# Optimization experiments

Measured on AMD Instinct MI355X. Metric: run time of the kernel, lower is better.

## Reference

```python
import jax, jax.numpy as jnp
import numpy as np

HALF_LOG_2PI = 0.9189385332046727  # 0.5*log(2*pi)


def _sum_layer(prod, logits):
    # prod: [B, R, KK] child log-probs; logits: [R, KK, K] unnormalized sum weights
    W = jax.nn.softmax(logits, axis=1)            # normalized mixture weights
    m = jnp.max(prod, axis=-1, keepdims=True)     # stable logsumexp via einsum
    e = jnp.exp(prod - m)                         # [B, R, KK]
    s = jnp.einsum('brc,rck->brk', e, W)          # [B, R, K]
    return jnp.log(s) + m


def setup_inputs() -> dict:
    key = jax.random.key(0)
    ks = jax.random.split(key, 12)
    B, F, K = 8192, 256, 8
    inp = {
        'x': jax.random.normal(ks[0], (B, F), dtype=jnp.float32),
        'mu': jax.random.normal(ks[1], (F, K), dtype=jnp.float32),
        'log_sigma': jax.random.uniform(ks[2], (F, K), dtype=jnp.float32),
    }
    R = F // 2
    for i in range(8):
        inp['w%d' % i] = jax.random.normal(ks[3 + i], (R, K * K, K), dtype=jnp.float32)
        R //= 2
    inp['root_w'] = jax.random.normal(ks[11], (K,), dtype=jnp.float32)
    return inp


def reference(x, mu, log_sigma, w0, w1, w2, w3, w4, w5, w6, w7, root_w):
    # Gaussian leaf log-probs: [B, F, K]
    z = (x[:, :, None] - mu) * jnp.exp(-log_sigma)
    h = -0.5 * z * z - log_sigma - HALF_LOG_2PI
    # Alternating product (pair adjacent regions) / sum (mix KK -> K) layers
    for w in (w0, w1, w2, w3, w4, w5, w6, w7):
        B, R, K = h.shape
        prod = (h[:, 0::2, :, None] + h[:, 1::2, None, :]).reshape(B, R // 2, K * K)
        h = _sum_layer(prod, w)
    # Root sum node over the K dists of the single remaining region -> [B]
    lp = h[:, 0, :] + jax.nn.log_softmax(root_w)
    return jax.scipy.special.logsumexp(lp, axis=-1)
```

## Files before the change

kernel.cpp:

```cpp
#include <hip/hip_runtime.h>
#include <math.h>

#define NTH 256

static constexpr float HLP = 0.9189385332046727f;

typedef __attribute__((ext_vector_type(2))) _Float16 half2v;
typedef __attribute__((ext_vector_type(2))) __fp16   fp16x2;

static constexpr int L1MF = 2097152;
static constexpr int L3NF = 2621440;
static constexpr int L3MF = 3145728;
static constexpr size_t WS_NEED_B = (size_t)3276800 * 4;

__device__ __forceinline__ half2v pkrtz(float a, float b) {
  return __builtin_bit_cast(half2v, __builtin_amdgcn_cvt_pkrtz(a, b));
}
__device__ __forceinline__ half2v u2h(unsigned u) {
  return __builtin_bit_cast(half2v, u);
}
__device__ __forceinline__ unsigned h2u(half2v h) {
  return __builtin_bit_cast(unsigned, h);
}
__device__ __forceinline__ float dd(half2v a, half2v b, float c) {
#if __has_builtin(__builtin_amdgcn_fdot2)
  return __builtin_amdgcn_fdot2(__builtin_bit_cast(fp16x2, a),
                                __builtin_bit_cast(fp16x2, b), c, false);
#else
  return fmaf((float)a[0], (float)b[0], fmaf((float)a[1], (float)b[1], c));
#endif
}
__device__ __forceinline__ float max8(const float* s) {
  float m = s[0];
  #pragma unroll
  for (int k = 1; k < 8; ++k) m = fmaxf(m, s[k]);
  return m;
}

__device__ __forceinline__ void leaf_ii(float xv, const float* mu8, const float* A8,
                                        const float* B8, half2v* ii, float* M) {
  float h[8];
  float m = -3.0e38f;
  #pragma unroll
  for (int k = 0; k < 8; ++k) {
    const float z = (xv - mu8[k]) * A8[k];
    h[k] = fmaf(-0.5f * z, z, B8[k]);
    m = fmaxf(m, h[k]);
  }
  #pragma unroll
  for (int k = 0; k < 8; ++k) {
    const float n = __expf(h[k] - m);
    ii[k] = pkrtz(n, n);
  }
  *M = m;
}
__device__ __forceinline__ void leaf_pk(float xv, const float* mu8, const float* A8,
                                        const float* B8, half2v* pk, float* M) {
  float h[8];
  float m = -3.0e38f;
  #pragma unroll
  for (int k = 0; k < 8; ++k) {
    const float z = (xv - mu8[k]) * A8[k];
    h[k] = fmaf(-0.5f * z, z, B8[k]);
    m = fmaxf(m, h[k]);
  }
  #pragma unroll
  for (int p = 0; p < 4; ++p) {
    const float n0 = __expf(h[2 * p] - m);
    const float n1 = __expf(h[2 * p + 1] - m);
    pk[p] = pkrtz(n0, n1);
  }
  *M = m;
}

template<int G, bool OUT_II>
__device__ __forceinline__ void combine_d2(const uint4* __restrict__ WL,
                                           const half2v (&na)[G][8],
                                           const half2v (&nb)[G][4],
                                           half2v (&oii)[G][8],
                                           half2v (&opk)[G][4],
                                           float (&M)[G]) {
  float s[G][8];
  #pragma unroll
  for (int g = 0; g < G; ++g)
    #pragma unroll
    for (int k = 0; k < 8; ++k) s[g][k] = 0.f;

  #pragma unroll
  for (int i = 0; i < 8; ++i) {
    half2v e[G][4];
    #pragma unroll
    for (int g = 0; g < G; ++g) {
      e[g][0] = na[g][i] * nb[g][0];
      e[g][1] = na[g][i] * nb[g][1];
      e[g][2] = na[g][i] * nb[g][2];
      e[g][3] = na[g][i] * nb[g][3];
    }
    #pragma unroll
    for (int k = 0; k < 8; ++k) {
      const uint4 w = WL[i * 8 + k];
      #pragma unroll
      for (int g = 0; g < G; ++g) {
        float acc = s[g][k];
        acc = dd(e[g][0], u2h(w.x), acc);
        acc = dd(e[g][1], u2h(w.y), acc);
        acc = dd(e[g][2], u2h(w.z), acc);
        acc = dd(e[g][3], u2h(w.w), acc);
        s[g][k] = acc;
      }
    }
  }
  #pragma unroll
  for (int g = 0; g < G; ++g) {
    const float smax = max8(s[g]);
    const float inv = 1.0f / smax;
    if constexpr (OUT_II) {
      #pragma unroll
      for (int p = 0; p < 8; ++p) {
        const float n = s[g][p] * inv;
        oii[g][p] = pkrtz(n, n);
      }
    } else {
      #pragma unroll
      for (int p = 0; p < 4; ++p)
        opk[g][p] = pkrtz(s[g][2 * p] * inv, s[g][2 * p + 1] * inv);
    }
    M[g] += __logf(smax);
  }
}

__device__ __forceinline__ void prep_col_std(const float* stage, unsigned* wdwL,
                                             int r, int k) {
  float v[64];
  float m = -3.0e38f;
  #pragma unroll
  for (int c = 0; c < 64; ++c) { v[c] = stage[r * 512 + c * 8 + k]; m = fmaxf(m, v[c]); }
  float t = 0.f;
  #pragma unroll
  for (int c = 0; c < 64; ++c) { v[c] = __expf(v[c] - m); t += v[c]; }
  const float inv = 1.0f / t;
  #pragma unroll
  for (int i = 0; i < 8; ++i)
    #pragma unroll
    for (int jp = 0; jp < 4; ++jp)
      wdwL[r * 256 + (i * 8 + k) * 4 + jp] =
          h2u(pkrtz(v[i * 8 + 2 * jp] * inv, v[i * 8 + 2 * jp + 1] * inv));
}

__global__ __launch_bounds__(NTH, 4) void spn_a(
    const float* __restrict__ x,
    const float* __restrict__ mu,
    const float* __restrict__ ls,
    const float* __restrict__ w0,
    const float* __restrict__ w1,
    float* __restrict__ ws)
{
  __shared__ float stage[1536];
  __shared__ uint4 wsh4[192];
  __shared__ float lsh[96];
  const int tid = threadIdx.x;
  const int r1 = blockIdx.x >> 4;
  const int chunk = blockIdx.x & 15;

  #pragma unroll
  for (int i = 0; i < 6; ++i) {
    const int idx = tid + 256 * i;
    const int reg = idx >> 9, off = idx & 511;
    const float* src = (reg == 0) ? (w0 + (2 * r1) * 512)
                     : (reg == 1) ? (w0 + (2 * r1 + 1) * 512)
                                  : (w1 + r1 * 512);
    stage[idx] = src[off];
  }
  if (tid < 96) {
    const int f8 = r1 * 32;
    if (tid < 32)      lsh[tid] = mu[f8 + tid];
    else if (tid < 64) lsh[tid] = __expf(-ls[f8 + (tid - 32)]);
    else               lsh[tid] = -ls[f8 + (tid - 64)] - HLP;
  }
  __syncthreads();

  if (tid < 24) prep_col_std(stage, reinterpret_cast<unsigned*>(wsh4), tid >> 3, tid & 7);
  __syncthreads();

  const int b0 = chunk * 512 + tid;
  const float4 xv0 = *reinterpret_cast<const float4*>(x + (size_t)b0 * 256 + 4 * r1);
  const float4 xv1 = *reinterpret_cast<const float4*>(x + (size_t)(b0 + 256) * 256 + 4 * r1);

  half2v ii[2][8], pk[2][4];
  half2v cAii[2][8], cBpk[2][4];
  half2v dmy_ii[2][8], dmy_pk[2][4];
  float MA[2], MB[2];
  float Ma, Mb;

  leaf_ii(xv0.x, lsh + 0, lsh + 32, lsh + 64, ii[0], &Ma);
  leaf_pk(xv0.y, lsh + 8, lsh + 40, lsh + 72, pk[0], &Mb);
  MA[0] = Ma + Mb;
  leaf_ii(xv1.x, lsh + 0, lsh + 32, lsh + 64, ii[1], &Ma);
  leaf_pk(xv1.y, lsh + 8, lsh + 40, lsh + 72, pk[1], &Mb);
  MA[1] = Ma + Mb;
  combine_d2<2, true>(wsh4, ii, pk, cAii, dmy_pk, MA);

  leaf_ii(xv0.z, lsh + 16, lsh + 48, lsh + 80, ii[0], &Ma);
  leaf_pk(xv0.w, lsh + 24, lsh + 56, lsh + 88, pk[0], &Mb);
  MB[0] = Ma + Mb;
  leaf_ii(xv1.z, lsh + 16, lsh + 48, lsh + 80, ii[1], &Ma);
  leaf_pk(xv1.w, lsh + 24, lsh + 56, lsh + 88, pk[1], &Mb);
  MB[1] = Ma + Mb;
  combine_d2<2, false>(wsh4 + 64, ii, pk, dmy_ii, cBpk, MB);

  float M[2] = {MA[0] + MB[0], MA[1] + MB[1]};
  half2v n[2][4];
  combine_d2<2, false>(wsh4 + 128, cAii, cBpk, dmy_ii, n, M);

  uint4* outn = reinterpret_cast<uint4*>(ws);
  outn[r1 * 8192 + b0]       = uint4{h2u(n[0][0]), h2u(n[0][1]), h2u(n[0][2]), h2u(n[0][3])};
  outn[r1 * 8192 + b0 + 256] = uint4{h2u(n[1][0]), h2u(n[1][1]), h2u(n[1][2]), h2u(n[1][3])};
  ws[L1MF + r1 * 8192 + b0]       = M[0];
  ws[L1MF + r1 * 8192 + b0 + 256] = M[1];
}

__device__ __forceinline__ void mk_ii(uint4 p, half2v* ii) {
  const half2v a0 = u2h(p.x), a1 = u2h(p.y), a2 = u2h(p.z), a3 = u2h(p.w);
  ii[0] = __builtin_shufflevector(a0, a0, 0, 0);
  ii[1] = __builtin_shufflevector(a0, a0, 1, 1);
  ii[2] = __builtin_shufflevector(a1, a1, 0, 0);
  ii[3] = __builtin_shufflevector(a1, a1, 1, 1);
  ii[4] = __builtin_shufflevector(a2, a2, 0, 0);
  ii[5] = __builtin_shufflevector(a2, a2, 1, 1);
  ii[6] = __builtin_shufflevector(a3, a3, 0, 0);
  ii[7] = __builtin_shufflevector(a3, a3, 1, 1);
}

__global__ __launch_bounds__(NTH, 4) void spn_b(
    const float* __restrict__ w2,
    const float* __restrict__ w3,
    float* __restrict__ ws)
{
  __shared__ float stage[1536];
  __shared__ uint4 wsh4[192];
  const int tid = threadIdx.x;
  const int r3 = blockIdx.x >> 5;
  const int chunk = blockIdx.x & 31;

  #pragma unroll
  for (int i = 0; i < 6; ++i) {
    const int idx = tid + 256 * i;
    const int reg = idx >> 9, off = idx & 511;
    const float* src = (reg == 0) ? (w2 + (2 * r3) * 512)
                     : (reg == 1) ? (w2 + (2 * r3 + 1) * 512)
                                  : (w3 + r3 * 512);
    stage[idx] = src[off];
  }
  __syncthreads();
  if (tid < 24) prep_col_std(stage, reinterpret_cast<unsigned*>(wsh4), tid >> 3, tid & 7);
  __syncthreads();

  const int b = chunk * 256 + tid;
  const uint4* n4 = reinterpret_cast<const uint4*>(ws);
  const uint4 p0 = n4[(4 * r3 + 0) * 8192 + b];
  const uint4 p1 = n4[(4 * r3 + 1) * 8192 + b];
  const uint4 p2 = n4[(4 * r3 + 2) * 8192 + b];
  const uint4 p3 = n4[(4 * r3 + 3) * 8192 + b];
  const float M0 = ws[L1MF + (4 * r3 + 0) * 8192 + b];
  const float M1 = ws[L1MF + (4 * r3 + 1) * 8192 + b];
  const float M2 = ws[L1MF + (4 * r3 + 2) * 8192 + b];
  const float M3 = ws[L1MF + (4 * r3 + 3) * 8192 + b];

  half2v ii[1][8], pk[1][4];
  half2v cAii[1][8], cBpk[1][4];
  half2v dmy_ii[1][8], dmy_pk[1][4];

  mk_ii(p0, ii[0]);
  pk[0][0] = u2h(p1.x); pk[0][1] = u2h(p1.y); pk[0][2] = u2h(p1.z); pk[0][3] = u2h(p1.w);
  float MA[1] = {M0 + M1};
  combine_d2<1, true>(wsh4, ii, pk, cAii, dmy_pk, MA);

  mk_ii(p2, ii[0]);
  pk[0][0] = u2h(p3.x); pk[0][1] = u2h(p3.y); pk[0][2] = u2h(p3.z); pk[0][3] = u2h(p3.w);
  float MB[1] = {M2 + M3};
  combine_d2<1, false>(wsh4 + 64, ii, pk, dmy_ii, cBpk, MB);

  float M[1] = {MA[0] + MB[0]};
  half2v n[1][4];
  combine_d2<1, false>(wsh4 + 128, cAii, cBpk, dmy_ii, n, M);

  reinterpret_cast<uint4*>(ws + L3NF)[r3 * 8192 + b] =
      uint4{h2u(n[0][0]), h2u(n[0][1]), h2u(n[0][2]), h2u(n[0][3])};
  ws[L3MF + r3 * 8192 + b] = M[0];
}

__device__ __forceinline__ float macTd(const uint4* __restrict__ Wr, int myk,
                                       const float* na, const half2v* nbpk) {
  float s = 0.f;
  #pragma unroll
  for (int i = 0; i < 8; ++i) {
    const uint4 w = Wr[myk * 8 + ((i ^ myk) & 7)];
    float T = dd(nbpk[0], u2h(w.x), 0.f);
    T = dd(nbpk[1], u2h(w.y), T);
    T = dd(nbpk[2], u2h(w.z), T);
    T = dd(nbpk[3], u2h(w.w), T);
    s = fmaf(na[i], T, s);
  }
  return s;
}

__global__ __launch_bounds__(NTH) void spn_c(
    const float* __restrict__ w4, const float* __restrict__ w5,
    const float* __restrict__ w6, const float* __restrict__ w7,
    const float* __restrict__ root_w,
    float* __restrict__ ws,
    float* __restrict__ out)
{
  __shared__ float stage[7680];
  __shared__ uint4 wsh4[960];
  __shared__ float ssh[8];
  const int tid = threadIdx.x;

  #pragma unroll
  for (int i = 0; i < 30; ++i) {
    const int idx = tid + 256 * i;
    const int reg = idx >> 9, off = idx & 511;
    const float* src;
    if (reg < 8)       src = w4 + reg * 512;
    else if (reg < 12) src = w5 + (reg - 8) * 512;
    else if (reg < 14) src = w6 + (reg - 12) * 512;
    else               src = w7;
    stage[idx] = src[off];
  }
  if (tid == 255) {
    float m = -3.0e38f;
    for (int k = 0; k < 8; ++k) m = fmaxf(m, root_w[k]);
    float e[8]; float t = 0.f;
    for (int k = 0; k < 8; ++k) { e[k] = __expf(root_w[k] - m); t += e[k]; }
    const float inv = 1.0f / t;
    for (int k = 0; k < 8; ++k) ssh[k] = e[k] * inv;
  }
  __syncthreads();

  if (tid < 120) {
    const int reg = tid >> 3, k = tid & 7;
    float v[64];
    float m = -3.0e38f;
    #pragma unroll
    for (int c = 0; c < 64; ++c) { v[c] = stage[reg * 512 + c * 8 + k]; m = fmaxf(m, v[c]); }
    float t = 0.f;
    #pragma unroll
    for (int c = 0; c < 64; ++c) { v[c] = __expf(v[c] - m); t += v[c]; }
    const float inv = 1.0f / t;
    unsigned* wdwL = reinterpret_cast<unsigned*>(wsh4);
    #pragma unroll
    for (int i = 0; i < 8; ++i)
      #pragma unroll
      for (int jp = 0; jp < 4; ++jp)
        wdwL[reg * 256 + k * 32 + (((i ^ k) & 7) << 2) + jp] =
            h2u(pkrtz(v[i * 8 + 2 * jp] * inv, v[i * 8 + 2 * jp + 1] * inv));
  }
  __syncthreads();

  const int lane = tid & 63, wid = tid >> 6;
  const int myk = lane & 7, bsub = lane >> 3, gbase = lane & 56;
  const int b = blockIdx.x * 32 + wid * 8 + bsub;

  const uint4* n4 = reinterpret_cast<const uint4*>(ws + L3NF);

  float n4v[8], M4[8];
  #pragma unroll
  for (int r = 0; r < 8; ++r) {
    const uint4 pa = n4[(2 * r + 0) * 8192 + b];
    const uint4 pb = n4[(2 * r + 1) * 8192 + b];
    const float Ma = ws[L3MF + (2 * r + 0) * 8192 + b];
    const float Mb = ws[L3MF + (2 * r + 1) * 8192 + b];
    float na[8];
    const half2v a0 = u2h(pa.x), a1 = u2h(pa.y), a2 = u2h(pa.z), a3 = u2h(pa.w);
    na[0] = (float)a0[0]; na[1] = (float)a0[1];
    na[2] = (float)a1[0]; na[3] = (float)a1[1];
    na[4] = (float)a2[0]; na[5] = (float)a2[1];
    na[6] = (float)a3[0]; na[7] = (float)a3[1];
    half2v nbpk[4] = {u2h(pb.x), u2h(pb.y), u2h(pb.z), u2h(pb.w)};
    float s = macTd(wsh4 + r * 64, myk, na, nbpk);
    float m = s;
    m = fmaxf(m, __shfl_xor(m, 1)); m = fmaxf(m, __shfl_xor(m, 2)); m = fmaxf(m, __shfl_xor(m, 4));
    n4v[r] = s / m;
    M4[r] = Ma + Mb + __logf(m);
  }

  float n5v[4], M5[4];
  #pragma unroll
  for (int r = 0; r < 4; ++r) {
    float na[8]; half2v nbpk[4];
    #pragma unroll
    for (int i = 0; i < 8; ++i) na[i] = __shfl(n4v[2 * r], gbase + i, 64);
    #pragma unroll
    for (int p = 0; p < 4; ++p)
      nbpk[p] = pkrtz(__shfl(n4v[2 * r + 1], gbase + 2 * p, 64),
                      __shfl(n4v[2 * r + 1], gbase + 2 * p + 1, 64));
    float s = macTd(wsh4 + (8 + r) * 64, myk, na, nbpk);
    float m = s;
    m = fmaxf(m, __shfl_xor(m, 1)); m = fmaxf(m, __shfl_xor(m, 2)); m = fmaxf(m, __shfl_xor(m, 4));
    n5v[r] = s / m;
    M5[r] = M4[2 * r] + M4[2 * r + 1] + __logf(m);
  }

  float n6v[2], M6[2];
  #pragma unroll
  for (int r = 0; r < 2; ++r) {
    float na[8]; half2v nbpk[4];
    #pragma unroll
    for (int i = 0; i < 8; ++i) na[i] = __shfl(n5v[2 * r], gbase + i, 64);
    #pragma unroll
    for (int p = 0; p < 4; ++p)
      nbpk[p] = pkrtz(__shfl(n5v[2 * r + 1], gbase + 2 * p, 64),
                      __shfl(n5v[2 * r + 1], gbase + 2 * p + 1, 64));
    float s = macTd(wsh4 + (12 + r) * 64, myk, na, nbpk);
    float m = s;
    m = fmaxf(m, __shfl_xor(m, 1)); m = fmaxf(m, __shfl_xor(m, 2)); m = fmaxf(m, __shfl_xor(m, 4));
    n6v[r] = s / m;
    M6[r] = M5[2 * r] + M5[2 * r + 1] + __logf(m);
  }

  {
    float na[8]; half2v nbpk[4];
    #pragma unroll
    for (int i = 0; i < 8; ++i) na[i] = __shfl(n6v[0], gbase + i, 64);
    #pragma unroll
    for (int p = 0; p < 4; ++p)
      nbpk[p] = pkrtz(__shfl(n6v[1], gbase + 2 * p, 64),
                      __shfl(n6v[1], gbase + 2 * p + 1, 64));
    float s = macTd(wsh4 + 14 * 64, myk, na, nbpk);
    float m = s;
    m = fmaxf(m, __shfl_xor(m, 1)); m = fmaxf(m, __shfl_xor(m, 2)); m = fmaxf(m, __shfl_xor(m, 4));
    const float n7 = s / m;
    const float M7 = M6[0] + M6[1] + __logf(m);
    float prod = n7 * ssh[myk];
    prod += __shfl_xor(prod, 1); prod += __shfl_xor(prod, 2); prod += __shfl_xor(prod, 4);
    if (myk == 0) out[b] = M7 + __logf(prod);
  }
}

static constexpr int NW   = 130560;
static constexpr int AOFF = NW;
static constexpr int BOFF = NW + 2048;
static constexpr int ROFF = NW + 4096;

__device__ __forceinline__ void leaf_eval(float xv, const float* mu8, const float* A8,
                                          const float* B8, float* n, float* M) {
  float h[8];
  float m = -3.0e38f;
  #pragma unroll
  for (int k = 0; k < 8; ++k) {
    const float z = (xv - mu8[k]) * A8[k];
    h[k] = fmaf(-0.5f * z, z, B8[k]);
    m = fmaxf(m, h[k]);
  }
  #pragma unroll
  for (int k = 0; k < 8; ++k) n[k] = __expf(h[k] - m);
  *M = m;
}

__global__ __launch_bounds__(256) void spn_prep(
    const float* __restrict__ ls,
    const float* __restrict__ w0, const float* __restrict__ w1,
    const float* __restrict__ w2, const float* __restrict__ w3,
    const float* __restrict__ w4, const float* __restrict__ w5,
    const float* __restrict__ w6, const float* __restrict__ w7,
    const float* __restrict__ root_w,
    float* __restrict__ ws)
{
  const int job = blockIdx.x * blockDim.x + threadIdx.x;
  if (job < 2040) {
    const float* wl[8] = {w0, w1, w2, w3, w4, w5, w6, w7};
    int j = job, l = 0, base = 0, R = 128;
    while (j >= R * 8) { j -= R * 8; base += R * 512; R >>= 1; ++l; }
    const int r = j >> 3, k = j & 7;
    const float* src = wl[l] + r * 512 + k;
    float v[64];
    float m = -3.0e38f;
    #pragma unroll
    for (int c = 0; c < 64; ++c) { v[c] = src[c * 8]; m = fmaxf(m, v[c]); }
    float ssum = 0.f;
    #pragma unroll
    for (int c = 0; c < 64; ++c) { v[c] = __expf(v[c] - m); ssum += v[c]; }
    const float inv = 1.0f / ssum;
    float* dst = ws + base + r * 512 + k;
    #pragma unroll
    for (int c = 0; c < 64; ++c) dst[c * 8] = v[c] * inv;
  } else if (job < 2040 + 2048) {
    const int i = job - 2040;
    const float l = ls[i];
    ws[AOFF + i] = __expf(-l);
    ws[BOFF + i] = -l - HLP;
  } else if (job == 2040 + 2048) {
    float m = -3.0e38f;
    for (int k = 0; k < 8; ++k) m = fmaxf(m, root_w[k]);
    float e[8]; float ssum = 0.f;
    for (int k = 0; k < 8; ++k) { e[k] = __expf(root_w[k] - m); ssum += e[k]; }
    const float inv = 1.0f / ssum;
    for (int k = 0; k < 8; ++k) ws[ROFF + k] = e[k] * inv;
  }
}

__device__ __forceinline__ void mac64(const float* __restrict__ Wr,
                                      const float* na, const float* nb,
                                      float* s) {
  #pragma unroll
  for (int k = 0; k < 8; ++k) s[k] = 0.f;
  #pragma unroll
  for (int i = 0; i < 8; ++i) {
    const float ai = na[i];
    #pragma unroll
    for (int j = 0; j < 8; ++j) {
      const float e = ai * nb[j];
      const float4 wA = *reinterpret_cast<const float4*>(Wr + (i * 8 + j) * 8);
      const float4 wB = *reinterpret_cast<const float4*>(Wr + (i * 8 + j) * 8 + 4);
      s[0] = fmaf(e, wA.x, s[0]); s[1] = fmaf(e, wA.y, s[1]);
      s[2] = fmaf(e, wA.z, s[2]); s[3] = fmaf(e, wA.w, s[3]);
      s[4] = fmaf(e, wB.x, s[4]); s[5] = fmaf(e, wB.y, s[5]);
      s[6] = fmaf(e, wB.z, s[6]); s[7] = fmaf(e, wB.w, s[7]);
    }
  }
}

#define TB 8
static constexpr int PLA = 128 * 9 + 5;
static constexpr int PLB = 64 * 9 + 5;
static constexpr int NAO = 0;
static constexpr int NBO = TB * PLA;
static constexpr int MAO = NBO + TB * PLB;
static constexpr int MBO = MAO + TB * 128;
static constexpr int SMEM_F = MBO + TB * 64;

__global__ __launch_bounds__(NTH, 2) void spn_main_fb(
    const float* __restrict__ x,
    const float* __restrict__ mu,
    const float* __restrict__ ws,
    float* __restrict__ out)
{
  const float* leafA = ws + AOFF;
  const float* leafB = ws + BOFF;
  const float* srw   = ws + ROFF;

  __shared__ float smem[SMEM_F];

  const int tid = threadIdx.x;
  const int bB = blockIdx.x * TB;

  {
    const float* W0 = ws;
    for (int it = tid; it < TB * 128; it += NTH) {
      const int bb = it & (TB - 1), r = it >> 3;
      float na[8], nb[8], Ma, Mb;
      const int f0 = 2 * r;
      const float xv0 = x[(bB + bb) * 256 + f0];
      const float xv1 = x[(bB + bb) * 256 + f0 + 1];
      leaf_eval(xv0, mu + f0 * 8, leafA + f0 * 8, leafB + f0 * 8, na, &Ma);
      leaf_eval(xv1, mu + f0 * 8 + 8, leafA + f0 * 8 + 8, leafB + f0 * 8 + 8, nb, &Mb);
      float s[8];
      mac64(W0 + r * 512, na, nb, s);
      const float smax = max8(s);
      const float inv = 1.0f / smax;
      const int ob = NAO + bb * PLA + r * 9;
      #pragma unroll
      for (int k = 0; k < 8; ++k) smem[ob + k] = s[k] * inv;
      smem[MAO + bb * 128 + r] = Ma + Mb + __logf(smax);
    }
  }
  __syncthreads();

  int pinO = NAO, poutO = NBO;
  int MinO = MAO, MoutO = MBO;
  int PLIN = PLA, PLOUT = PLB;
  int Rin = 128;
  const float* Wl = ws + 128 * 512;
  for (int l = 1; l < 7; ++l) {
    const int Rout = Rin >> 1;
    for (int it = tid; it < TB * Rout; it += NTH) {
      const int bb = it & (TB - 1), r = it >> 3;
      float na[8], nb[8];
      const int ia = pinO + bb * PLIN + (2 * r) * 9;
      #pragma unroll
      for (int i = 0; i < 8; ++i) { na[i] = smem[ia + i]; nb[i] = smem[ia + 9 + i]; }
      float s[8];
      mac64(Wl + r * 512, na, nb, s);
      const float smax = max8(s);
      const float inv = 1.0f / smax;
      const int ob = poutO + bb * PLOUT + r * 9;
      #pragma unroll
      for (int k = 0; k < 8; ++k) smem[ob + k] = s[k] * inv;
      smem[MoutO + bb * Rout + r] =
          smem[MinO + bb * Rin + 2 * r] + smem[MinO + bb * Rin + 2 * r + 1] + __logf(smax);
    }
    __syncthreads();
    int t;
    t = pinO; pinO = poutO; poutO = t;
    t = MinO; MinO = MoutO; MoutO = t;
    t = PLIN; PLIN = PLOUT; PLOUT = t;
    Rin = Rout;
    Wl += Rout * 512;
  }

  for (int it = tid; it < TB; it += NTH) {
    const int bb = it;
    float na[8], nb[8];
    const int ia = pinO + bb * PLIN;
    #pragma unroll
    for (int i = 0; i < 8; ++i) { na[i] = smem[ia + i]; nb[i] = smem[ia + 9 + i]; }
    float s[8];
    mac64(Wl, na, nb, s);
    float acc = 0.f;
    #pragma unroll
    for (int k = 0; k < 8; ++k) acc = fmaf(s[k], srw[k], acc);
    out[bB + bb] = smem[MinO + bb * 2] + smem[MinO + bb * 2 + 1] + __logf(acc);
  }
}

extern "C" void kernel_launch(void* const* d_in, const int* in_sizes, int n_in,
                              void* d_out, int out_size, void* d_ws, size_t ws_size,
                              hipStream_t stream) {
  (void)in_sizes; (void)n_in; (void)out_size;
  const float* x      = (const float*)d_in[0];
  const float* mu     = (const float*)d_in[1];
  const float* ls     = (const float*)d_in[2];
  const float* w0     = (const float*)d_in[3];
  const float* w1     = (const float*)d_in[4];
  const float* w2     = (const float*)d_in[5];
  const float* w3     = (const float*)d_in[6];
  const float* w4     = (const float*)d_in[7];
  const float* w5     = (const float*)d_in[8];
  const float* w6     = (const float*)d_in[9];
  const float* w7     = (const float*)d_in[10];
  const float* root_w = (const float*)d_in[11];
  float* ws  = (float*)d_ws;
  float* out = (float*)d_out;

  if (ws_size >= WS_NEED_B) {
    spn_a<<<1024, NTH, 0, stream>>>(x, mu, ls, w0, w1, ws);
    spn_b<<<512, NTH, 0, stream>>>(w2, w3, ws);
    spn_c<<<256, NTH, 0, stream>>>(w4, w5, w6, w7, root_w, ws, out);
  } else {
    spn_prep<<<16, 256, 0, stream>>>(ls, w0, w1, w2, w3, w4, w5, w6, w7, root_w, ws);
    spn_main_fb<<<8192 / TB, NTH, 0, stream>>>(x, mu, ws, out);
  }
}
```

Baseline: 51.75 us.

## Fuse leaf and first four SPN layers into one kernel to drop intermediate round-trip

Merges the spn_a and spn_b kernels into spn_ab, where each thread evaluates a 16-feature subtree from the leaves up through layer 3 entirely in registers. This removes the layer-1 intermediate write and read in global memory plus one kernel launch, and shrinks the workspace. In exchange each block stages and softmax-normalises 15 weight regions instead of 3, so it uses more shared memory and more serial prep. The launch bound drops to 2 blocks per SM and the grid is halved, so occupancy and the parallelism of the prep phase fall.

```diff
diff --git a/kernel.cpp b/kernel.cpp
--- a/kernel.cpp
+++ b/kernel.cpp
@@ -8,10 +8,8 @@
 typedef __attribute__((ext_vector_type(2))) _Float16 half2v;
 typedef __attribute__((ext_vector_type(2))) __fp16   fp16x2;
 
-static constexpr int L1MF = 2097152;
-static constexpr int L3NF = 2621440;
-static constexpr int L3MF = 3145728;
-static constexpr size_t WS_NEED_B = (size_t)3276800 * 4;
+static constexpr int L3MF = 524288;
+static constexpr size_t WS_NEED_B = (size_t)655360 * 4;
 
 __device__ __forceinline__ half2v pkrtz(float a, float b) {
   return __builtin_bit_cast(half2v, __builtin_amdgcn_cvt_pkrtz(a, b));
@@ -147,144 +145,98 @@
           h2u(pkrtz(v[i * 8 + 2 * jp] * inv, v[i * 8 + 2 * jp + 1] * inv));
 }
 
-__global__ __launch_bounds__(NTH, 4) void spn_a(
+template<bool OUT_II>
+__device__ __forceinline__ void subtree_eval(const uint4* __restrict__ wsh4, int sub,
+                                             const float* lsh, float4 xv,
+                                             half2v (&oii)[1][8], half2v (&opk)[1][4],
+                                             float* Mout) {
+  half2v ii[1][8], pk[1][4];
+  half2v aii[1][8], bpk[1][4];
+  half2v dii[1][8], dpk[1][4];
+  float Ma, Mb;
+  const int fl = 4 * sub;
+
+  leaf_ii(xv.x, lsh + fl * 8,       lsh + 128 + fl * 8,       lsh + 256 + fl * 8,       ii[0], &Ma);
+  leaf_pk(xv.y, lsh + (fl + 1) * 8, lsh + 128 + (fl + 1) * 8, lsh + 256 + (fl + 1) * 8, pk[0], &Mb);
+  float MA[1] = {Ma + Mb};
+  combine_d2<1, true>(wsh4 + (2 * sub) * 64, ii, pk, aii, dpk, MA);
+
+  leaf_ii(xv.z, lsh + (fl + 2) * 8, lsh + 128 + (fl + 2) * 8, lsh + 256 + (fl + 2) * 8, ii[0], &Ma);
+  leaf_pk(xv.w, lsh + (fl + 3) * 8, lsh + 128 + (fl + 3) * 8, lsh + 256 + (fl + 3) * 8, pk[0], &Mb);
+  float MB[1] = {Ma + Mb};
+  combine_d2<1, false>(wsh4 + (2 * sub + 1) * 64, ii, pk, dii, bpk, MB);
+
+  float M[1] = {MA[0] + MB[0]};
+  combine_d2<1, OUT_II>(wsh4 + (8 + sub) * 64, aii, bpk, oii, opk, M);
+  *Mout = M[0];
+}
+
+__global__ __launch_bounds__(NTH, 2) void spn_ab(
     const float* __restrict__ x,
     const float* __restrict__ mu,
     const float* __restrict__ ls,
-    const float* __restrict__ w0,
-    const float* __restrict__ w1,
+    const float* __restrict__ w0, const float* __restrict__ w1,
+    const float* __restrict__ w2, const float* __restrict__ w3,
     float* __restrict__ ws)
 {
-  __shared__ float stage[1536];
-  __shared__ uint4 wsh4[192];
-  __shared__ float lsh[96];
-  const int tid = threadIdx.x;
-  const int r1 = blockIdx.x >> 4;
-  const int chunk = blockIdx.x & 15;
-
-  #pragma unroll
-  for (int i = 0; i < 6; ++i) {
-    const int idx = tid + 256 * i;
-    const int reg = idx >> 9, off = idx & 511;
-    const float* src = (reg == 0) ? (w0 + (2 * r1) * 512)
-                     : (reg == 1) ? (w0 + (2 * r1 + 1) * 512)
-                                  : (w1 + r1 * 512);
-    stage[idx] = src[off];
-  }
-  if (tid < 96) {
-    const int f8 = r1 * 32;
-    if (tid < 32)      lsh[tid] = mu[f8 + tid];
-    else if (tid < 64) lsh[tid] = __expf(-ls[f8 + (tid - 32)]);
-    else               lsh[tid] = -ls[f8 + (tid - 64)] - HLP;
-  }
-  __syncthreads();
-
-  if (tid < 24) prep_col_std(stage, reinterpret_cast<unsigned*>(wsh4), tid >> 3, tid & 7);
-  __syncthreads();
-
-  const int b0 = chunk * 512 + tid;
-  const float4 xv0 = *reinterpret_cast<const float4*>(x + (size_t)b0 * 256 + 4 * r1);
-  const float4 xv1 = *reinterpret_cast<const float4*>(x + (size_t)(b0 + 256) * 256 + 4 * r1);
-
-  half2v ii[2][8], pk[2][4];
-  half2v cAii[2][8], cBpk[2][4];
-  half2v dmy_ii[2][8], dmy_pk[2][4];
-  float MA[2], MB[2];
-  float Ma, Mb;
-
-  leaf_ii(xv0.x, lsh + 0, lsh + 32, lsh + 64, ii[0], &Ma);
-  leaf_pk(xv0.y, lsh + 8, lsh + 40, lsh + 72, pk[0], &Mb);
-  MA[0] = Ma + Mb;
-  leaf_ii(xv1.x, lsh + 0, lsh + 32, lsh + 64, ii[1], &Ma);
-  leaf_pk(xv1.y, lsh + 8, lsh + 40, lsh + 72, pk[1], &Mb);
-  MA[1] = Ma + Mb;
-  combine_d2<2, true>(wsh4, ii, pk, cAii, dmy_pk, MA);
-
-  leaf_ii(xv0.z, lsh + 16, lsh + 48, lsh + 80, ii[0], &Ma);
-  leaf_pk(xv0.w, lsh + 24, lsh + 56, lsh + 88, pk[0], &Mb);
-  MB[0] = Ma + Mb;
-  leaf_ii(xv1.z, lsh + 16, lsh + 48, lsh + 80, ii[1], &Ma);
-  leaf_pk(xv1.w, lsh + 24, lsh + 56, lsh + 88, pk[1], &Mb);
-  MB[1] = Ma + Mb;
-  combine_d2<2, false>(wsh4 + 64, ii, pk, dmy_ii, cBpk, MB);
-
-  float M[2] = {MA[0] + MB[0], MA[1] + MB[1]};
-  half2v n[2][4];
-  combine_d2<2, false>(wsh4 + 128, cAii, cBpk, dmy_ii, n, M);
-
-  uint4* outn = reinterpret_cast<uint4*>(ws);
-  outn[r1 * 8192 + b0]       = uint4{h2u(n[0][0]), h2u(n[0][1]), h2u(n[0][2]), h2u(n[0][3])};
-  outn[r1 * 8192 + b0 + 256] = uint4{h2u(n[1][0]), h2u(n[1][1]), h2u(n[1][2]), h2u(n[1][3])};
-  ws[L1MF + r1 * 8192 + b0]       = M[0];
-  ws[L1MF + r1 * 8192 + b0 + 256] = M[1];
-}
-
-__device__ __forceinline__ void mk_ii(uint4 p, half2v* ii) {
-  const half2v a0 = u2h(p.x), a1 = u2h(p.y), a2 = u2h(p.z), a3 = u2h(p.w);
-  ii[0] = __builtin_shufflevector(a0, a0, 0, 0);
-  ii[1] = __builtin_shufflevector(a0, a0, 1, 1);
-  ii[2] = __builtin_shufflevector(a1, a1, 0, 0);
-  ii[3] = __builtin_shufflevector(a1, a1, 1, 1);
-  ii[4] = __builtin_shufflevector(a2, a2, 0, 0);
-  ii[5] = __builtin_shufflevector(a2, a2, 1, 1);
-  ii[6] = __builtin_shufflevector(a3, a3, 0, 0);
-  ii[7] = __builtin_shufflevector(a3, a3, 1, 1);
-}
-
-__global__ __launch_bounds__(NTH, 4) void spn_b(
-    const float* __restrict__ w2,
-    const float* __restrict__ w3,
-    float* __restrict__ ws)
-{
-  __shared__ float stage[1536];
-  __shared__ uint4 wsh4[192];
+  __shared__ float stage[7680];
+  __shared__ uint4 wsh4[960];
+  __shared__ float lsh[384];
   const int tid = threadIdx.x;
   const int r3 = blockIdx.x >> 5;
   const int chunk = blockIdx.x & 31;
 
   #pragma unroll
-  for (int i = 0; i < 6; ++i) {
+  for (int i = 0; i < 30; ++i) {
     const int idx = tid + 256 * i;
     const int reg = idx >> 9, off = idx & 511;
-    const float* src = (reg == 0) ? (w2 + (2 * r3) * 512)
-                     : (reg == 1) ? (w2 + (2 * r3 + 1) * 512)
-                                  : (w3 + r3 * 512);
+    const float* src;
+    if (reg < 8)       src = w0 + (8 * r3 + reg) * 512;
+    else if (reg < 12) src = w1 + (4 * r3 + (reg - 8)) * 512;
+    else if (reg < 14) src = w2 + (2 * r3 + (reg - 12)) * 512;
+    else               src = w3 + r3 * 512;
     stage[idx] = src[off];
   }
+  if (tid < 128) {
+    const int base = r3 * 128;
+    const float l = ls[base + tid];
+    lsh[tid]       = mu[base + tid];
+    lsh[128 + tid] = __expf(-l);
+    lsh[256 + tid] = -l - HLP;
+  }
   __syncthreads();
-  if (tid < 24) prep_col_std(stage, reinterpret_cast<unsigned*>(wsh4), tid >> 3, tid & 7);
+
+  if (tid < 120) prep_col_std(stage, reinterpret_cast<unsigned*>(wsh4), tid >> 3, tid & 7);
   __syncthreads();
 
   const int b = chunk * 256 + tid;
-  const uint4* n4 = reinterpret_cast<const uint4*>(ws);
-  const uint4 p0 = n4[(4 * r3 + 0) * 8192 + b];
-  const uint4 p1 = n4[(4 * r3 + 1) * 8192 + b];
-  const uint4 p2 = n4[(4 * r3 + 2) * 8192 + b];
-  const uint4 p3 = n4[(4 * r3 + 3) * 8192 + b];
-  const float M0 = ws[L1MF + (4 * r3 + 0) * 8192 + b];
-  const float M1 = ws[L1MF + (4 * r3 + 1) * 8192 + b];
-  const float M2 = ws[L1MF + (4 * r3 + 2) * 8192 + b];
-  const float M3 = ws[L1MF + (4 * r3 + 3) * 8192 + b];
-
-  half2v ii[1][8], pk[1][4];
-  half2v cAii[1][8], cBpk[1][4];
-  half2v dmy_ii[1][8], dmy_pk[1][4];
-
-  mk_ii(p0, ii[0]);
-  pk[0][0] = u2h(p1.x); pk[0][1] = u2h(p1.y); pk[0][2] = u2h(p1.z); pk[0][3] = u2h(p1.w);
+  const float* xb = x + (size_t)b * 256 + 16 * r3;
+  const float4 xv0 = *reinterpret_cast<const float4*>(xb);
+  const float4 xv1 = *reinterpret_cast<const float4*>(xb + 4);
+  const float4 xv2 = *reinterpret_cast<const float4*>(xb + 8);
+  const float4 xv3 = *reinterpret_cast<const float4*>(xb + 12);
+
+  half2v s0ii[1][8], s1pk[1][4], s2ii[1][8], s3pk[1][4];
+  half2v dii[1][8], dpk[1][4];
+  float M0, M1, M2, M3;
+
+  subtree_eval<true >(wsh4, 0, lsh, xv0, s0ii, dpk, &M0);
+  subtree_eval<false>(wsh4, 1, lsh, xv1, dii, s1pk, &M1);
   float MA[1] = {M0 + M1};
-  combine_d2<1, true>(wsh4, ii, pk, cAii, dmy_pk, MA);
-
-  mk_ii(p2, ii[0]);
-  pk[0][0] = u2h(p3.x); pk[0][1] = u2h(p3.y); pk[0][2] = u2h(p3.z); pk[0][3] = u2h(p3.w);
+  half2v cAii[1][8];
+  combine_d2<1, true>(wsh4 + 12 * 64, s0ii, s1pk, cAii, dpk, MA);
+
+  subtree_eval<true >(wsh4, 2, lsh, xv2, s2ii, dpk, &M2);
+  subtree_eval<false>(wsh4, 3, lsh, xv3, dii, s3pk, &M3);
   float MB[1] = {M2 + M3};
-  combine_d2<1, false>(wsh4 + 64, ii, pk, dmy_ii, cBpk, MB);
+  half2v cBpk[1][4];
+  combine_d2<1, false>(wsh4 + 13 * 64, s2ii, s3pk, dii, cBpk, MB);
 
   float M[1] = {MA[0] + MB[0]};
   half2v n[1][4];
-  combine_d2<1, false>(wsh4 + 128, cAii, cBpk, dmy_ii, n, M);
-
-  reinterpret_cast<uint4*>(ws + L3NF)[r3 * 8192 + b] =
+  combine_d2<1, false>(wsh4 + 14 * 64, cAii, cBpk, dii, n, M);
+
+  reinterpret_cast<uint4*>(ws)[r3 * 8192 + b] =
       uint4{h2u(n[0][0]), h2u(n[0][1]), h2u(n[0][2]), h2u(n[0][3])};
   ws[L3MF + r3 * 8192 + b] = M[0];
 }
@@ -361,7 +313,7 @@
   const int myk = lane & 7, bsub = lane >> 3, gbase = lane & 56;
   const int b = blockIdx.x * 32 + wid * 8 + bsub;
 
-  const uint4* n4 = reinterpret_cast<const uint4*>(ws + L3NF);
+  const uint4* n4 = reinterpret_cast<const uint4*>(ws);
 
   float n4v[8], M4[8];
   #pragma unroll
@@ -633,8 +585,7 @@
   float* out = (float*)d_out;
 
   if (ws_size >= WS_NEED_B) {
-    spn_a<<<1024, NTH, 0, stream>>>(x, mu, ls, w0, w1, ws);
-    spn_b<<<512, NTH, 0, stream>>>(w2, w3, ws);
+    spn_ab<<<512, NTH, 0, stream>>>(x, mu, ls, w0, w1, w2, w3, ws);
     spn_c<<<256, NTH, 0, stream>>>(w4, w5, w6, w7, root_w, ws, out);
   } else {
     spn_prep<<<16, 256, 0, stream>>>(ls, w0, w1, w2, w3, w4, w5, w6, w7, root_w, ws);
```

Result: faster. 50.68 us (-2.1%).
